# Optimization experiments

Hardware: AMD Instinct MI355X
Metric: run time of the kernel (lower is better)

## Reference

```python
import jax, jax.numpy as jnp
import numpy as np

K_NEIGHBORS = 3
CLASSES = 5


def _l2_norm(x):
    # x: (N, C, H, W) -> (N, H*W, C), unit L2 norm over channel dim
    N, C, H, W = x.shape
    x = x.reshape(N, C, H * W).transpose(0, 2, 1)
    return x / jnp.linalg.norm(x, axis=-1, keepdims=True)


def setup_inputs() -> dict:
    key = jax.random.key(0)
    k1, k2 = jax.random.split(key)
    anchor = jax.random.normal(k1, (32, 64, 21, 21), dtype=jnp.float32)
    support_set = jax.random.normal(k2, (25, 64, 21, 21), dtype=jnp.float32)
    return {"anchor": anchor, "support_set": support_set, "av_num": 1, "sav_num": 1}


def reference(anchor, support_set, av_num, sav_num):
    # anchor: (B*AV, C, H, W), support_set: (L*S, C, H, W)
    q = _l2_norm(anchor)            # (B, HW, C)
    s = _l2_norm(support_set)       # (L*S, HW, C)
    C = s.shape[-1]
    s_flat = s.reshape(-1, C)       # (M, C), M = L*S*HW (class-major)
    # dense cosine similarity: (B, HW, M)
    sim = jnp.einsum('bqc,mc->bqm', q, s_flat)
    B, HW, M = sim.shape
    per_cls = M // CLASSES
    # (B//av, av, HW, L, S*HW)
    sim = sim.reshape(B // av_num, av_num, HW, CLASSES, per_cls)
    sim = jax.nn.sigmoid(sim)
    # av_num == 1 -> squeeze AV dim (matches torch squeeze(1) path)
    sim = sim[:, 0] if av_num == 1 else jnp.power(jnp.prod(sim, axis=1), 1.0 / av_num)
    # per-class top-k over descriptors, sum over k and over query locations
    topk = jax.lax.top_k(sim, K_NEIGHBORS)[0]        # (B, HW, L, K)
    i2c_sim = topk.sum(axis=-1).sum(axis=-2)         # (B, L)
    return i2c_sim
```

## Files before the change

### kernel.cpp

```cpp
#include <hip/hip_runtime.h>
#include <hip/hip_bf16.h>
#include <math.h>

#define CLASSES     5
#define C_DIM       64
#define HW          441
#define B_ANCH      32
#define NSUP        25
#define NROWS       (B_ANCH*HW)
#define MSUP        (NSUP*HW)
#define PER_CLS     (MSUP/CLASSES)
#define TILE_COLS   32
#define ROW_BYTES   (C_DIM*2)
#define TILE_BYTES  (TILE_COLS*ROW_BYTES)
#define PER_CLS_PAD 2304
#define NPAD        (PER_CLS_PAD - PER_CLS)
#define QUARTERS    4
#define TILES_PER_Q 18
#define ROWS_PER_BLK 128
#define NBLK_X      ((NROWS + ROWS_PER_BLK - 1) / ROWS_PER_BLK)

#define NEG_INF  (-1e30f)

typedef __bf16 bf16x8 __attribute__((ext_vector_type(8)));
typedef float  f32x4  __attribute__((ext_vector_type(4)));

#define TOP3_INS(v, t0, t1, t2) do {                              \
    float _v = (v);                                               \
    float _n0 = fmaxf(_v, (t0));                                  \
    float _n1 = __builtin_amdgcn_fmed3f(_v, (t0), (t1));          \
    float _n2 = __builtin_amdgcn_fmed3f(_v, (t1), (t2));          \
    (t0) = _n0; (t1) = _n1; (t2) = _n2; } while (0)

#define TRIPLE_MERGE(u0, u1, u2, v0, v1, v2) do {                 \
    float _A = fminf((u0), (v0));                                 \
    float _B = fmaxf((u1), (v1));                                 \
    float _E = fmaxf((u2), (v2));                                 \
    float _m0 = fmaxf((u0), (v0));                                \
    float _m1 = __builtin_amdgcn_fmed3f((u0), (v0), _B);          \
    float _m2 = __builtin_amdgcn_fmed3f(_A, _B, _E);              \
    (u0) = _m0; (u1) = _m1; (u2) = _m2; } while (0)

typedef __attribute__((address_space(1))) const void g_void;
typedef __attribute__((address_space(3))) void l_void;
__device__ __forceinline__ void gload_lds16(const void* g, void* l) {
    __builtin_amdgcn_global_load_lds((g_void*)g, (l_void*)l, 16, 0, 0);
}
#define MFMA16(A, B, C) __builtin_amdgcn_mfma_f32_16x16x32_bf16((A), (B), (C), 0, 0, 0)

__global__ __launch_bounds__(256) void norm_rows_kernel(
    const float* __restrict__ anchor, const float* __restrict__ support,
    __bf16* __restrict__ qb, __bf16* __restrict__ sb) {
    int r = blockIdx.x * 256 + threadIdx.x;
    const int total_main = MSUP + NROWS;
    if (r >= total_main) {
        int i = r - total_main;
        if (i < CLASSES * NPAD) {
            int cls = i / NPAD, ix = PER_CLS + i % NPAD;
            __bf16* op = sb + ((size_t)cls * PER_CLS_PAD + ix) * C_DIM;
            bf16x8 z = {};
            #pragma unroll
            for (int c0 = 0; c0 < C_DIM; c0 += 8) *(bf16x8*)(op + c0) = z;
        }
        return;
    }
    bool isSup = r < MSUP;
    int rc = isSup ? r : r - MSUP;
    const float* in = isSup ? support : anchor;
    int img = rc / HW, p = rc % HW;
    const float* base = in + (size_t)img * C_DIM * HW + p;
    float q[C_DIM];
    float ss = 0.f;
    #pragma unroll
    for (int c = 0; c < C_DIM; ++c) { q[c] = base[c * HW]; ss += q[c] * q[c]; }
    float sc = rsqrtf(ss);
    __bf16* op;
    if (isSup) {
        int cls = rc / PER_CLS, ix = rc - cls * PER_CLS;
        op = sb + ((size_t)cls * PER_CLS_PAD + ix) * C_DIM;
    } else {
        op = qb + (size_t)rc * C_DIM;
    }
    #pragma unroll
    for (int c0 = 0; c0 < C_DIM; c0 += 8) {
        bf16x8 v;
        #pragma unroll
        for (int j = 0; j < 8; ++j) v[j] = (__bf16)(q[c0 + j] * sc);
        *(bf16x8*)(op + c0) = v;
    }
}

template<int QNT, bool TAIL>
__device__ __forceinline__ void gemm_quarter(
    const char* stage_src, char* smem_base, const char* pB,
    int xoff0, int xoff1, int stage_dst_off, int lane, int kg,
    const bf16x8 q0h0, const bf16x8 q0h1, const bf16x8 q1h0, const bf16x8 q1h1,
    float u0[2], float u1[2], float u2[2]) {

    auto stage = [&](int buf, int tt) {
        gload_lds16(stage_src + tt * TILE_BYTES,
                    smem_base + buf * 4096 + stage_dst_off);
    };
    const f32x4 z = {0.f, 0.f, 0.f, 0.f};
    stage(0, 0);
    stage(1, 1);
    #pragma unroll
    for (int tt = 0; tt < QNT; ++tt) {
        if (tt < QNT - 1) asm volatile("s_waitcnt vmcnt(1)" ::: "memory");
        else              asm volatile("s_waitcnt vmcnt(0)" ::: "memory");
        __builtin_amdgcn_s_barrier();
        if (tt + 2 < QNT) stage((tt + 2) % 3, tt + 2);
        const int buf = tt % 3;
        const bool tail = TAIL && (tt == QNT - 1);
        const char* pb = pB + buf * 4096;
        bf16x8 a0h0 = *(const bf16x8*)(pb + xoff0);
        bf16x8 a0h1 = *(const bf16x8*)(pb + xoff1);
        bf16x8 a1h0 = *(const bf16x8*)(pb + 2048 + xoff0);
        bf16x8 a1h1 = *(const bf16x8*)(pb + 2048 + xoff1);
        f32x4 acc00, acc01, acc10, acc11;
        __builtin_amdgcn_s_setprio(1);
        acc00 = MFMA16(a0h0, q0h0, z);    acc00 = MFMA16(a0h1, q0h1, acc00);
        acc01 = MFMA16(a0h0, q1h0, z);    acc01 = MFMA16(a0h1, q1h1, acc01);
        acc10 = MFMA16(a1h0, q0h0, z);    acc10 = MFMA16(a1h1, q0h1, acc10);
        acc11 = MFMA16(a1h0, q1h0, z);    acc11 = MFMA16(a1h1, q1h1, acc11);
        __builtin_amdgcn_s_setprio(0);
        if (!tail) {
            #pragma unroll
            for (int j = 0; j < 4; ++j) {
                TOP3_INS(acc00[j], u0[0], u1[0], u2[0]);
                TOP3_INS(acc01[j], u0[1], u1[1], u2[1]);
                TOP3_INS(acc10[j], u0[0], u1[0], u2[0]);
                TOP3_INS(acc11[j], u0[1], u1[1], u2[1]);
            }
        } else {
            #pragma unroll
            for (int j = 0; j < 4; ++j) {
                TOP3_INS(acc00[j], u0[0], u1[0], u2[0]);
                TOP3_INS(acc01[j], u0[1], u1[1], u2[1]);
                bool validj = (j == 0) || (kg < 3);
                float v0 = validj ? acc10[j] : NEG_INF;
                float v1 = validj ? acc11[j] : NEG_INF;
                TOP3_INS(v0, u0[0], u1[0], u2[0]);
                TOP3_INS(v1, u0[1], u1[1], u2[1]);
            }
        }
    }
}

__global__ __launch_bounds__(256, 4) void knn_mfma_kernel(
    const __bf16* __restrict__ qb, const __bf16* __restrict__ sb,
    float* __restrict__ part) {
    __shared__ char smem[3][4096];

    int lane = threadIdx.x & 63;
    int w    = threadIdx.x >> 6;
    int lr   = lane & 15;
    int kg   = lane >> 4;
    int cls  = blockIdx.y >> 2;
    int q    = blockIdx.y & 3;
    int rowbase = blockIdx.x * ROWS_PER_BLK + w * 32;

    int r0 = rowbase + lr;       r0 = r0 < NROWS ? r0 : NROWS - 1;
    int r1 = rowbase + 16 + lr;  r1 = r1 < NROWS ? r1 : NROWS - 1;
    const bf16x8* qr0 = (const bf16x8*)(qb + (size_t)r0 * C_DIM);
    const bf16x8* qr1 = (const bf16x8*)(qb + (size_t)r1 * C_DIM);
    bf16x8 q0h0 = qr0[kg], q0h1 = qr0[4 + kg];
    bf16x8 q1h0 = qr1[kg], q1h1 = qr1[4 + kg];

    float u0[2], u1[2], u2[2];
    #pragma unroll
    for (int f = 0; f < 2; ++f) { u0[f] = NEG_INF; u1[f] = NEG_INF; u2[f] = NEG_INF; }

    int srow = lane >> 3;
    int sgrn = (lane & 7) ^ (srow & 7);
    int srcSwz = srow * 128 + sgrn * 16;
    const char* qbase = (const char*)sb
        + (size_t)cls * PER_CLS_PAD * ROW_BYTES
        + (size_t)q * TILES_PER_Q * TILE_BYTES;
    const char* stage_src = qbase + w * 1024 + srcSwz;
    int xoff0 = (((lr & 7) ^ kg) << 4);
    int xoff1 = xoff0 ^ 0x40;
    const char* pB = (const char*)smem + lr * 128;

    if (q == 3)
        gemm_quarter<15, true >(stage_src, (char*)smem, pB, xoff0, xoff1,
                                w * 1024, lane, kg,
                                q0h0, q0h1, q1h0, q1h1, u0, u1, u2);
    else
        gemm_quarter<18, false>(stage_src, (char*)smem, pB, xoff0, xoff1,
                                w * 1024, lane, kg,
                                q0h0, q0h1, q1h0, q1h1, u0, u1, u2);

    #pragma unroll
    for (int f = 0; f < 2; ++f) {
        float a0 = u0[f], a1 = u1[f], a2 = u2[f];
        #pragma unroll
        for (int off = 16; off < 64; off <<= 1) {
            float v0 = __shfl_xor(a0, off, 64);
            float v1 = __shfl_xor(a1, off, 64);
            float v2 = __shfl_xor(a2, off, 64);
            TRIPLE_MERGE(a0, a1, a2, v0, v1, v2);
        }
        int row = rowbase + f * 16 + lr;
        if (kg == 0 && row < NROWS) {
            float* pp = part +
                ((size_t)(row * CLASSES + cls) * QUARTERS + q) * 3;
            pp[0] = a0; pp[1] = a1; pp[2] = a2;
        }
    }
}

__global__ __launch_bounds__(64) void merge_reduce_kernel(
    const float* __restrict__ part, float* __restrict__ out) {
    int bl = blockIdx.x;
    int b = bl / CLASSES;
    int l = bl % CLASSES;
    int lane = threadIdx.x;
    float acc = 0.f;
    for (int p = lane; p < HW; p += 64) {
        int row = b * HW + p;
        const float* pp = part + (size_t)(row * CLASSES + l) * (QUARTERS * 3);
        float u0 = pp[0], u1 = pp[1], u2 = pp[2];
        TRIPLE_MERGE(u0, u1, u2, pp[3], pp[4],  pp[5]);
        TRIPLE_MERGE(u0, u1, u2, pp[6], pp[7],  pp[8]);
        TRIPLE_MERGE(u0, u1, u2, pp[9], pp[10], pp[11]);
        acc += 1.f / (1.f + __expf(-u0))
             + 1.f / (1.f + __expf(-u1))
             + 1.f / (1.f + __expf(-u2));
    }
    #pragma unroll
    for (int off = 32; off; off >>= 1) acc += __shfl_xor(acc, off, 64);
    if (lane == 0) out[bl] = acc;
}

extern "C" void kernel_launch(void* const* d_in, const int* in_sizes, int n_in,
                              void* d_out, int out_size, void* d_ws, size_t ws_size,
                              hipStream_t stream) {
    const float* anchor  = (const float*)d_in[0];
    const float* support = (const float*)d_in[1];

    __bf16* sb = (__bf16*)d_ws;
    __bf16* qb = sb + (size_t)CLASSES * PER_CLS_PAD * C_DIM;
    float* part = (float*)(qb + (size_t)NROWS * C_DIM);

    {
        int total = MSUP + NROWS + CLASSES * NPAD;
        dim3 g((total + 255) / 256);
        norm_rows_kernel<<<g, 256, 0, stream>>>(anchor, support, qb, sb);
    }
    {
        dim3 g(NBLK_X, CLASSES * QUARTERS);
        knn_mfma_kernel<<<g, 256, 0, stream>>>(qb, sb, part);
    }
    {
        dim3 gm(B_ANCH * CLASSES);
        merge_reduce_kernel<<<gm, 64, 0, stream>>>(part, (float*)d_out);
    }
}
```

Before: 48.05 us.

## Replace LDS-staged support tiles with direct register triple-buffered global loads

```diff
diff --git a/kernel.cpp b/kernel.cpp
--- a/kernel.cpp
+++ b/kernel.cpp
@@ -41,11 +41,6 @@
     float _m2 = __builtin_amdgcn_fmed3f(_A, _B, _E);              \
     (u0) = _m0; (u1) = _m1; (u2) = _m2; } while (0)
 
-typedef __attribute__((address_space(1))) const void g_void;
-typedef __attribute__((address_space(3))) void l_void;
-__device__ __forceinline__ void gload_lds16(const void* g, void* l) {
-    __builtin_amdgcn_global_load_lds((g_void*)g, (l_void*)l, 16, 0, 0);
-}
 #define MFMA16(A, B, C) __builtin_amdgcn_mfma_f32_16x16x32_bf16((A), (B), (C), 0, 0, 0)
 
 __global__ __launch_bounds__(256) void norm_rows_kernel(
@@ -91,39 +86,31 @@
 }
 
 template<int QNT, bool TAIL>
-__device__ __forceinline__ void gemm_quarter(
-    const char* stage_src, char* smem_base, const char* pB,
-    int xoff0, int xoff1, int stage_dst_off, int lane, int kg,
-    const bf16x8 q0h0, const bf16x8 q0h1, const bf16x8 q1h0, const bf16x8 q1h1,
+__device__ __forceinline__ void scan_quarter(
+    const char* abase,
+    int kg,
+    const bf16x8 qh0[2], const bf16x8 qh1[2],
     float u0[2], float u1[2], float u2[2]) {
 
-    auto stage = [&](int buf, int tt) {
-        gload_lds16(stage_src + tt * TILE_BYTES,
-                    smem_base + buf * 4096 + stage_dst_off);
+    bf16x8 A[4], B[4], C[4];
+    auto load = [&](bf16x8 d[4], int t) {
+        const char* p = abase + t * TILE_BYTES;
+        d[0] = *(const bf16x8*)(p);
+        d[1] = *(const bf16x8*)(p + 64);
+        d[2] = *(const bf16x8*)(p + 2048);
+        d[3] = *(const bf16x8*)(p + 2048 + 64);
     };
     const f32x4 z = {0.f, 0.f, 0.f, 0.f};
-    stage(0, 0);
-    stage(1, 1);
-    #pragma unroll
-    for (int tt = 0; tt < QNT; ++tt) {
-        if (tt < QNT - 1) asm volatile("s_waitcnt vmcnt(1)" ::: "memory");
-        else              asm volatile("s_waitcnt vmcnt(0)" ::: "memory");
-        __builtin_amdgcn_s_barrier();
-        if (tt + 2 < QNT) stage((tt + 2) % 3, tt + 2);
-        const int buf = tt % 3;
-        const bool tail = TAIL && (tt == QNT - 1);
-        const char* pb = pB + buf * 4096;
-        bf16x8 a0h0 = *(const bf16x8*)(pb + xoff0);
-        bf16x8 a0h1 = *(const bf16x8*)(pb + xoff1);
-        bf16x8 a1h0 = *(const bf16x8*)(pb + 2048 + xoff0);
-        bf16x8 a1h1 = *(const bf16x8*)(pb + 2048 + xoff1);
+
+    auto comp = [&](const bf16x8 s[4], int t) {
         f32x4 acc00, acc01, acc10, acc11;
         __builtin_amdgcn_s_setprio(1);
-        acc00 = MFMA16(a0h0, q0h0, z);    acc00 = MFMA16(a0h1, q0h1, acc00);
-        acc01 = MFMA16(a0h0, q1h0, z);    acc01 = MFMA16(a0h1, q1h1, acc01);
-        acc10 = MFMA16(a1h0, q0h0, z);    acc10 = MFMA16(a1h1, q0h1, acc10);
-        acc11 = MFMA16(a1h0, q1h0, z);    acc11 = MFMA16(a1h1, q1h1, acc11);
+        acc00 = MFMA16(s[0], qh0[0], z); acc00 = MFMA16(s[1], qh1[0], acc00);
+        acc01 = MFMA16(s[0], qh0[1], z); acc01 = MFMA16(s[1], qh1[1], acc01);
+        acc10 = MFMA16(s[2], qh0[0], z); acc10 = MFMA16(s[3], qh1[0], acc10);
+        acc11 = MFMA16(s[2], qh0[1], z); acc11 = MFMA16(s[3], qh1[1], acc11);
         __builtin_amdgcn_s_setprio(0);
+        const bool tail = TAIL && (t == QNT - 1);
         if (!tail) {
             #pragma unroll
             for (int j = 0; j < 4; ++j) {
@@ -144,14 +131,23 @@
                 TOP3_INS(v1, u0[1], u1[1], u2[1]);
             }
         }
+    };
+
+    load(A, 0);
+    load(B, 1);
+    #pragma unroll
+    for (int t = 0; t < QNT; ++t) {
+        switch (t % 3) {
+            case 0:  if (t + 2 < QNT) load(C, t + 2); comp(A, t); break;
+            case 1:  if (t + 2 < QNT) load(A, t + 2); comp(B, t); break;
+            default: if (t + 2 < QNT) load(B, t + 2); comp(C, t); break;
+        }
     }
 }
 
 __global__ __launch_bounds__(256, 4) void knn_mfma_kernel(
     const __bf16* __restrict__ qb, const __bf16* __restrict__ sb,
     float* __restrict__ part) {
-    __shared__ char smem[3][4096];
-
     int lane = threadIdx.x & 63;
     int w    = threadIdx.x >> 6;
     int lr   = lane & 15;
@@ -160,36 +156,29 @@
     int q    = blockIdx.y & 3;
     int rowbase = blockIdx.x * ROWS_PER_BLK + w * 32;
 
-    int r0 = rowbase + lr;       r0 = r0 < NROWS ? r0 : NROWS - 1;
-    int r1 = rowbase + 16 + lr;  r1 = r1 < NROWS ? r1 : NROWS - 1;
-    const bf16x8* qr0 = (const bf16x8*)(qb + (size_t)r0 * C_DIM);
-    const bf16x8* qr1 = (const bf16x8*)(qb + (size_t)r1 * C_DIM);
-    bf16x8 q0h0 = qr0[kg], q0h1 = qr0[4 + kg];
-    bf16x8 q1h0 = qr1[kg], q1h1 = qr1[4 + kg];
+    bf16x8 qh0[2], qh1[2];
+    #pragma unroll
+    for (int f = 0; f < 2; ++f) {
+        int r = rowbase + f * 16 + lr;
+        r = r < NROWS ? r : NROWS - 1;
+        const bf16x8* qr = (const bf16x8*)(qb + (size_t)r * C_DIM);
+        qh0[f] = qr[kg];
+        qh1[f] = qr[4 + kg];
+    }
 
     float u0[2], u1[2], u2[2];
     #pragma unroll
     for (int f = 0; f < 2; ++f) { u0[f] = NEG_INF; u1[f] = NEG_INF; u2[f] = NEG_INF; }
 
-    int srow = lane >> 3;
-    int sgrn = (lane & 7) ^ (srow & 7);
-    int srcSwz = srow * 128 + sgrn * 16;
-    const char* qbase = (const char*)sb
+    const char* abase = (const char*)sb
         + (size_t)cls * PER_CLS_PAD * ROW_BYTES
-        + (size_t)q * TILES_PER_Q * TILE_BYTES;
-    const char* stage_src = qbase + w * 1024 + srcSwz;
-    int xoff0 = (((lr & 7) ^ kg) << 4);
-    int xoff1 = xoff0 ^ 0x40;
-    const char* pB = (const char*)smem + lr * 128;
+        + (size_t)q * TILES_PER_Q * TILE_BYTES
+        + lr * ROW_BYTES + kg * 16;
 
     if (q == 3)
-        gemm_quarter<15, true >(stage_src, (char*)smem, pB, xoff0, xoff1,
-                                w * 1024, lane, kg,
-                                q0h0, q0h1, q1h0, q1h1, u0, u1, u2);
+        scan_quarter<15, true >(abase, kg, qh0, qh1, u0, u1, u2);
     else
-        gemm_quarter<18, false>(stage_src, (char*)smem, pB, xoff0, xoff1,
-                                w * 1024, lane, kg,
-                                q0h0, q0h1, q1h0, q1h1, u0, u1, u2);
+        scan_quarter<18, false>(abase, kg, qh0, qh1, u0, u1, u2);
 
     #pragma unroll
     for (int f = 0; f < 2; ++f) {
@@ -204,7 +193,7 @@
         int row = rowbase + f * 16 + lr;
         if (kg == 0 && row < NROWS) {
             float* pp = part +
-                ((size_t)(row * CLASSES + cls) * QUARTERS + q) * 3;
+                (((size_t)cls * NROWS + row) * QUARTERS + q) * 3;
             pp[0] = a0; pp[1] = a1; pp[2] = a2;
         }
     }
@@ -219,7 +208,7 @@
     float acc = 0.f;
     for (int p = lane; p < HW; p += 64) {
         int row = b * HW + p;
-        const float* pp = part + (size_t)(row * CLASSES + l) * (QUARTERS * 3);
+        const float* pp = part + (((size_t)l * NROWS + row) * QUARTERS) * 3;
         float u0 = pp[0], u1 = pp[1], u2 = pp[2];
         TRIPLE_MERGE(u0, u1, u2, pp[3], pp[4],  pp[5]);
         TRIPLE_MERGE(u0, u1, u2, pp[6], pp[7],  pp[8]);
```

Result: slower. 91.96 us (+91.4%).
